# Kernel optimization log

Measured on AMD Instinct MI355X. Metric: run time of the kernel, lower is better.

Reference implementation:

```python
import jax, jax.numpy as jnp
import numpy as np

B, T, C = 8, 2048, 1024
HEAD_SIZE = 64
HEAD_NUM = 0
NUM_HEADS = 16


def setup_inputs() -> dict:
    key = jax.random.key(0)
    k1, k2, k3, k4 = jax.random.split(key, 4)
    x = jax.random.normal(k1, (B, T, C), dtype=jnp.float32)
    s = C ** -0.5  # Linear init scale
    Wq = jax.random.normal(k2, (C, HEAD_SIZE), dtype=jnp.float32) * s
    Wk = jax.random.normal(k3, (C, HEAD_SIZE), dtype=jnp.float32) * s
    Wv = jax.random.normal(k4, (C, HEAD_SIZE), dtype=jnp.float32) * s
    return {"x": x, "Wq": Wq, "Wk": Wk, "Wv": Wv}


def reference(x, Wq, Wk, Wv):
    # single head of self-attention with ALiBi bias + causal mask (dropout in eval mode = identity)
    q = x @ Wq  # [B,T,H]
    k = x @ Wk  # [B,T,H]
    v = x @ Wv  # [B,T,H]
    scale = jnp.float32(HEAD_SIZE) ** -0.5
    t = jnp.arange(T)
    # base_bias[i,j] = j - i, scaled by per-head ALiBi slope
    slope = 2.0 ** (-8.0 * (HEAD_NUM + 1) / NUM_HEADS)
    m = (t[None, :] - t[:, None]).astype(jnp.float32) * slope  # [T,T]
    # note: bias is added BEFORE the 1/sqrt(d) scaling, as in the original
    scores = (jnp.einsum('bqh,bkh->bqk', q, k) + m) * scale  # [B,T,T]
    causal = t[None, :] <= t[:, None]  # [T,T] lower-triangular
    scores = jnp.where(causal, scores, -jnp.inf)
    attn = jax.nn.softmax(scores, axis=-1)
    out = jnp.einsum('bqk,bkh->bqh', attn, v)  # [B,T,H]
    return out
```

## Files before the change

### kernel.cpp

```cpp
#include <hip/hip_runtime.h>
#include <hip/hip_bf16.h>
#include <math.h>

#define B_ 8
#define T_ 2048
#define C_ 1024
#define H_ 64
#define M_ (B_*T_)

typedef __attribute__((ext_vector_type(8))) short bf16x8;
typedef __attribute__((ext_vector_type(4))) float floatx4;

static __device__ __forceinline__ unsigned short f2bf(float f) {
    union { float f; unsigned u; } v; v.f = f;
    unsigned r = v.u + 0x7fffu + ((v.u >> 16) & 1u);
    return (unsigned short)(r >> 16);
}
static __device__ __forceinline__ unsigned short f2bf_fast(float f) {
    union { float f; unsigned u; } v; v.f = f;
    return (unsigned short)((v.u + 0x8000u) >> 16);
}
static __device__ __forceinline__ unsigned pk2h(float lo, float hi) {
    union { float f; unsigned u; } a, b; a.f = lo; b.f = hi;
    return __builtin_amdgcn_perm(b.u + 0x8000u, a.u + 0x8000u, 0x07060302u);
}
static __device__ __forceinline__ bf16x8 cvt8(float4 f0, float4 f1) {
    union { uint4 u; bf16x8 v; } r;
    r.u.x = pk2h(f0.x, f0.y); r.u.y = pk2h(f0.z, f0.w);
    r.u.z = pk2h(f1.x, f1.y); r.u.w = pk2h(f1.z, f1.w);
    return r.v;
}
static __device__ __forceinline__ float fexp2(float x) {
#if defined(__has_builtin)
#if __has_builtin(__builtin_amdgcn_exp2f)
    return __builtin_amdgcn_exp2f(x);
#else
    return exp2f(x);
#endif
#else
    return exp2f(x);
#endif
}

#define MFMA(a,b,c) __builtin_amdgcn_mfma_f32_16x16x32_bf16((a),(b),(c),0,0,0)

__global__ __launch_bounds__(256) void wprep_kernel(
    const float* __restrict__ Wq, const float* __restrict__ Wk,
    const float* __restrict__ Wv, unsigned short* __restrict__ wt2)
{
    const int f    = blockIdx.x * 256 + threadIdx.x;
    const int nt   = f >> 11;
    const int kc   = (f >> 6) & 31;
    const int lane = f & 63;
    const int l15  = lane & 15, quad = lane >> 4;
    const int col  = nt * 16 + l15;
    const float* W = (col < 64) ? Wq : ((col < 128) ? Wk : Wv);
    const int   cw = col & 63;
    const float sc = (col < 64) ? 0.125f : 1.0f;
    unsigned short o[8];
    #pragma unroll
    for (int j = 0; j < 8; j++) {
        const int kk = kc * 32 + quad * 8 + j;
        o[j] = f2bf(W[(size_t)kk * 64 + cw] * sc);
    }
    *(uint4*)&wt2[(size_t)f * 8] = *(const uint4*)o;
}

__global__ __launch_bounds__(256) void qkv_kernel(
    const float* __restrict__ x, const unsigned short* __restrict__ wt2,
    unsigned short* __restrict__ qo, unsigned short* __restrict__ ko,
    unsigned short* __restrict__ vo)
{
    __shared__ __align__(16) unsigned short smem[32 * 200];
    #define XS_(buf) (smem + (buf) * 2304)

    const int t    = threadIdx.x;
    const int w    = t >> 6;
    const int lane = t & 63;
    const int l15  = lane & 15;
    const int quad = lane >> 4;
    const int r0   = blockIdx.x * 32;

    const int srow = t >> 3;
    const int g0   = t & 7;
    const float* xrow = x + (size_t)(r0 + srow) * C_;

    const unsigned short* wb = wt2 + (size_t)(w * 3) * 32 * 512 + lane * 8;

    floatx4 acc[2][3];
    #pragma unroll
    for (int mt = 0; mt < 2; mt++)
        #pragma unroll
        for (int nt = 0; nt < 3; nt++) acc[mt][nt] = (floatx4)(0.0f);

    float4 xA[2], xB[2];
    bf16x8 wcur[6], wnxt[6];

    xA[0] = *(const float4*)(xrow + g0 * 8);
    xA[1] = *(const float4*)(xrow + g0 * 8 + 4);
    xB[0] = *(const float4*)(xrow + 64 + g0 * 8);
    xB[1] = *(const float4*)(xrow + 64 + g0 * 8 + 4);
    #pragma unroll
    for (int nt = 0; nt < 3; nt++)
        #pragma unroll
        for (int ks = 0; ks < 2; ks++)
            wcur[nt * 2 + ks] = *(const bf16x8*)(wb + (size_t)(nt * 32 + ks) * 512);
    *(bf16x8*)(XS_(0) + srow * 72 + g0 * 8) = cvt8(xA[0], xA[1]);
    __syncthreads();

    #define QSTEP(c, Xcur, Xnext, buf)                                         \
    {                                                                          \
        if ((c) < 14) {                                                        \
            const int k2 = ((c) + 2) * 64;                                     \
            Xcur[0] = *(const float4*)(xrow + k2 + g0 * 8);                    \
            Xcur[1] = *(const float4*)(xrow + k2 + g0 * 8 + 4);                \
        }                                                                      \
        if ((c) < 15) {                                                        \
            _Pragma("unroll")                                                  \
            for (int nt = 0; nt < 3; nt++)                                     \
                _Pragma("unroll")                                              \
                for (int ks = 0; ks < 2; ks++)                                 \
                    wnxt[nt * 2 + ks] = *(const bf16x8*)                       \
                        (wb + (size_t)(nt * 32 + 2 * ((c) + 1) + ks) * 512);   \
        }                                                                      \
        _Pragma("unroll")                                                      \
        for (int ks = 0; ks < 2; ks++) {                                       \
            bf16x8 af[2];                                                      \
            _Pragma("unroll")                                                  \
            for (int mt = 0; mt < 2; mt++)                                     \
                af[mt] = *(const bf16x8*)                                      \
                    (XS_(buf) + (mt * 16 + l15) * 72 + ks * 32 + quad * 8);    \
            _Pragma("unroll")                                                  \
            for (int mt = 0; mt < 2; mt++)                                     \
                _Pragma("unroll")                                              \
                for (int nt = 0; nt < 3; nt++)                                 \
                    acc[mt][nt] = MFMA(af[mt], wcur[nt * 2 + ks], acc[mt][nt]);\
        }                                                                      \
        if ((c) < 15) {                                                        \
            *(bf16x8*)(XS_((buf) ^ 1) + srow * 72 + g0 * 8)                    \
                = cvt8(Xnext[0], Xnext[1]);                                    \
            _Pragma("unroll")                                                  \
            for (int i = 0; i < 6; i++) wcur[i] = wnxt[i];                     \
        }                                                                      \
        __syncthreads();                                                       \
    }

    for (int cc = 0; cc < 16; cc += 2) {
        QSTEP(cc,     xA, xB, 0)
        QSTEP(cc + 1, xB, xA, 1)
    }
    #undef QSTEP

    #pragma unroll
    for (int mt = 0; mt < 2; mt++)
        #pragma unroll
        for (int nt = 0; nt < 3; nt++) {
            const int col = w * 48 + nt * 16 + l15;
            #pragma unroll
            for (int r = 0; r < 4; r++)
                smem[(mt * 16 + quad * 4 + r) * 200 + col] = f2bf(acc[mt][nt][r]);
        }
    __syncthreads();

    {
        const int row = t >> 3;
        const int oct = t & 7;
        *(uint4*)&qo[(size_t)(r0 + row) * 64 + oct * 8] =
            *(const uint4*)&smem[row * 200 + oct * 8];
        *(uint4*)&ko[(size_t)(r0 + row) * 64 + oct * 8] =
            *(const uint4*)&smem[row * 200 + 64 + oct * 8];
    }
    {
        const int h = t >> 2, ts = (t & 3) * 8;
        const int bb = r0 >> 11, tt = r0 & 2047;
        unsigned short tmp[8];
        #pragma unroll
        for (int j = 0; j < 8; j++) tmp[j] = smem[(ts + j) * 200 + 128 + h];
        *(uint4*)&vo[((size_t)bb * 64 + h) * 2048 + tt + ts] = *(uint4*)&tmp[0];
    }
    #undef XS_
}

#define L2E 1.4426950408889634f
#define BS2 0.12751743f

__global__ __launch_bounds__(256, 2) void attn_kernel(
    const unsigned short* __restrict__ q,
    const unsigned short* __restrict__ k,
    const unsigned short* __restrict__ vT,
    float* __restrict__ out)
{
    __shared__ __align__(16) unsigned char smem[32768 + 1024];
    unsigned short* pT  = (unsigned short*)smem;
    float*          Omg = (float*)smem;
    float*          mlg = (float*)(smem + 32768);

    const int t    = threadIdx.x;
    const int w    = t >> 6;
    const int lane = t & 63;
    const int l15  = lane & 15;
    const int quad = lane >> 4;
    const int b    = blockIdx.x & 7;
    const int qt   = 63 - (blockIdx.x >> 3);
    const int q0   = qt * 32;
    const size_t kb = (size_t)b * T_ * 64;

    bf16x8 qf[2][2];
    #pragma unroll
    for (int rt = 0; rt < 2; rt++)
        #pragma unroll
        for (int ks = 0; ks < 2; ks++)
            qf[rt][ks] = *(const bf16x8*)
                &q[kb + (size_t)(q0 + rt * 16 + l15) * 64 + ks * 32 + quad * 8];

    floatx4 O[2][4];
    float mrow[2][4], lrow[2][4];
    #pragma unroll
    for (int rt = 0; rt < 2; rt++) {
        #pragma unroll
        for (int nt = 0; nt < 4; nt++) O[rt][nt] = (floatx4)(0.0f);
        #pragma unroll
        for (int r = 0; r < 4; r++) { mrow[rt][r] = -INFINITY; lrow[rt][r] = 0.0f; }
    }

    const int nsteps = (q0 + 32 + 63) >> 6;
    const int ns4    = (nsteps + 3) >> 2;
    const int sBeg   = w * ns4;
    const int sEnd   = min(sBeg + ns4, nsteps);
    unsigned short* pw = pT + w * 32 * 72;

    bf16x8 kf[4][2], vf[4][2];
    #define LOADK(dK, jj0)                                                     \
        { _Pragma("unroll")                                                    \
          for (int nt = 0; nt < 4; nt++)                                       \
              _Pragma("unroll")                                                \
              for (int ks = 0; ks < 2; ks++)                                   \
                  dK[nt][ks] = *(const bf16x8*)                                \
                      &k[kb + (size_t)((jj0) + nt*16 + l15)*64 + ks*32 + quad*8]; }
    #define LOADV(dV, jj0)                                                     \
        { _Pragma("unroll")                                                    \
          for (int nt = 0; nt < 4; nt++)                                       \
              _Pragma("unroll")                                                \
              for (int ks = 0; ks < 2; ks++)                                   \
                  dV[nt][ks] = *(const bf16x8*)                                \
                      &vT[((size_t)b*64 + nt*16 + l15)*2048 + (jj0) + ks*32 + quad*8]; }

    #define SMPART(MASKED)                                                     \
    {                                                                          \
        _Pragma("unroll")                                                      \
        for (int rt = 0; rt < 2; rt++)                                         \
            _Pragma("unroll")                                                  \
            for (int r = 0; r < 4; r++) {                                      \
                float xv[4];                                                   \
                _Pragma("unroll")                                              \
                for (int nt = 0; nt < 4; nt++) {                               \
                    float v2 = fmaf(sc[rt][nt][r], L2E, jn[nt]);               \
                    if (MASKED) {                                              \
                        const int ig = q0 + rt * 16 + quad * 4 + r;            \
                        if (j0 + nt * 16 + l15 > ig) v2 = -INFINITY;           \
                    }                                                          \
                    xv[nt] = v2;                                               \
                }                                                              \
                float mloc = fmaxf(fmaxf(xv[0], xv[1]), fmaxf(xv[2], xv[3]));  \
                _Pragma("unroll")                                              \
                for (int off = 1; off < 16; off <<= 1)                         \
                    mloc = fmaxf(mloc, __shfl_xor(mloc, off));                 \
                const float mnew  = fmaxf(mrow[rt][r], mloc);                  \
                const float alpha = fexp2(mrow[rt][r] - mnew);                 \
                mrow[rt][r] = mnew;                                            \
                float ps = 0.0f;                                               \
                _Pragma("unroll")                                              \
                for (int nt = 0; nt < 4; nt++) {                               \
                    const float p = fexp2(xv[nt] - mnew);                      \
                    ps += p;                                                   \
                    pw[(rt * 16 + quad * 4 + r) * 72 + nt * 16 + l15]          \
                        = f2bf_fast(p);                                        \
                }                                                              \
                lrow[rt][r] = lrow[rt][r] * alpha + ps;                        \
                _Pragma("unroll")                                              \
                for (int nt = 0; nt < 4; nt++) O[rt][nt][r] *= alpha;          \
            }                                                                  \
    }

    if (sBeg < sEnd) LOADK(kf, sBeg * 64)

    for (int s = sBeg; s < sEnd; s++) {
        const int j0 = s * 64;

        floatx4 sc[2][4];
        #pragma unroll
        for (int rt = 0; rt < 2; rt++)
            #pragma unroll
            for (int nt = 0; nt < 4; nt++) {
                floatx4 z = (floatx4)(0.0f);
                z = MFMA(qf[rt][0], kf[nt][0], z);
                z = MFMA(qf[rt][1], kf[nt][1], z);
                sc[rt][nt] = z;
            }

        LOADV(vf, j0)
        bf16x8 kf2[4][2];
        const bool more = (s + 1 < sEnd);
        if (more) LOADK(kf2, (s + 1) * 64)

        const float jb = (float)(j0 + l15) * BS2;
        const float jn[4] = { jb, jb + 16.0f * BS2, jb + 32.0f * BS2,
                              jb + 48.0f * BS2 };
        if (s != nsteps - 1) SMPART(false) else SMPART(true);

        #pragma unroll
        for (int rt = 0; rt < 2; rt++) {
            const bf16x8 pf0 = *(const bf16x8*)&pw[(rt * 16 + l15) * 72 + quad * 8];
            const bf16x8 pf1 = *(const bf16x8*)&pw[(rt * 16 + l15) * 72 + 32 + quad * 8];
            #pragma unroll
            for (int nt = 0; nt < 4; nt++) {
                O[rt][nt] = MFMA(pf0, vf[nt][0], O[rt][nt]);
                O[rt][nt] = MFMA(pf1, vf[nt][1], O[rt][nt]);
            }
        }

        if (more) {
            #pragma unroll
            for (int nt = 0; nt < 4; nt++)
                #pragma unroll
                for (int ks = 0; ks < 2; ks++)
                    kf[nt][ks] = kf2[nt][ks];
        }
    }
    #undef LOADK
    #undef LOADV
    #undef SMPART

    #pragma unroll
    for (int rt = 0; rt < 2; rt++)
        #pragma unroll
        for (int r = 0; r < 4; r++)
            #pragma unroll
            for (int off = 1; off < 16; off <<= 1)
                lrow[rt][r] += __shfl_xor(lrow[rt][r], off);

    __syncthreads();

    #pragma unroll
    for (int rt = 0; rt < 2; rt++)
        #pragma unroll
        for (int nt = 0; nt < 4; nt++)
            #pragma unroll
            for (int r = 0; r < 4; r++)
                Omg[w * 2048 + (rt * 16 + quad * 4 + r) * 64 + nt * 16 + l15]
                    = O[rt][nt][r];
    if (l15 == 0) {
        #pragma unroll
        for (int rt = 0; rt < 2; rt++)
            #pragma unroll
            for (int r = 0; r < 4; r++) {
                mlg[w * 64 + rt * 16 + quad * 4 + r]      = mrow[rt][r];
                mlg[w * 64 + 32 + rt * 16 + quad * 4 + r] = lrow[rt][r];
            }
    }
    __syncthreads();

    {
        const int row = t >> 3;
        const int hq  = (t & 7) << 3;
        float mstar = -INFINITY;
        #pragma unroll
        for (int w2 = 0; w2 < 4; w2++)
            mstar = fmaxf(mstar, mlg[w2 * 64 + row]);
        floatx4 oa0 = (floatx4)(0.0f), oa1 = (floatx4)(0.0f);
        float lsum = 0.0f;
        #pragma unroll
        for (int w2 = 0; w2 < 4; w2++) {
            const float wg = fexp2(mlg[w2 * 64 + row] - mstar);
            lsum += wg * mlg[w2 * 64 + 32 + row];
            oa0 += wg * *(const floatx4*)&Omg[w2 * 2048 + row * 64 + hq];
            oa1 += wg * *(const floatx4*)&Omg[w2 * 2048 + row * 64 + hq + 4];
        }
        const float inv = 1.0f / lsum;
        *(floatx4*)&out[kb + (size_t)(q0 + row) * 64 + hq]     = oa0 * inv;
        *(floatx4*)&out[kb + (size_t)(q0 + row) * 64 + hq + 4] = oa1 * inv;
    }
}

extern "C" void kernel_launch(void* const* d_in, const int* in_sizes, int n_in,
                              void* d_out, int out_size, void* d_ws, size_t ws_size,
                              hipStream_t stream) {
    (void)in_sizes; (void)n_in; (void)out_size; (void)ws_size;
    const float* x  = (const float*)d_in[0];
    const float* Wq = (const float*)d_in[1];
    const float* Wk = (const float*)d_in[2];
    const float* Wv = (const float*)d_in[3];
    float* out = (float*)d_out;

    unsigned short* wt2 = (unsigned short*)d_ws;
    unsigned short* qw  = wt2 + 196608;
    unsigned short* kw  = qw + (size_t)M_ * H_;
    unsigned short* vw  = kw + (size_t)M_ * H_;

    wprep_kernel<<<96, 256, 0, stream>>>(Wq, Wk, Wv, wt2);
    qkv_kernel<<<M_ / 32, 256, 0, stream>>>(x, wt2, qw, kw, vw);
    attn_kernel<<<B_ * 64, 256, 0, stream>>>(qw, kw, vw, out);
}
```

Baseline: 137.3 us.

## Stage full x tile in LDS for QKV and halve attention query tile

The QKV projection now loads and converts the block's entire 32x1024 x tile into LDS up front, in an MFMA-fragment-friendly layout. This removes the per-chunk double buffering and the per-chunk barriers from the inner loop, at the cost of 64KB of LDS per block and less overlap between loads and compute. The attention kernel now uses 16-row query tiles instead of 32, doubling the grid to 1024 blocks. It also shrinks LDS, raises the occupancy hint to 3, pads the P stride to 76, and drops the separate K prefetch registers to lower register pressure. In exchange, each block does less work per K/V load, so global reuse is lower.

```diff
diff --git a/kernel.cpp b/kernel.cpp
--- a/kernel.cpp
+++ b/kernel.cpp
@@ -71,8 +71,7 @@
     unsigned short* __restrict__ qo, unsigned short* __restrict__ ko,
     unsigned short* __restrict__ vo)
 {
-    __shared__ __align__(16) unsigned short smem[32 * 200];
-    #define XS_(buf) (smem + (buf) * 2304)
+    __shared__ __align__(16) unsigned short smem[32768];
 
     const int t    = threadIdx.x;
     const int w    = t >> 6;
@@ -81,9 +80,30 @@
     const int quad = lane >> 4;
     const int r0   = blockIdx.x * 32;
 
-    const int srow = t >> 3;
-    const int g0   = t & 7;
-    const float* xrow = x + (size_t)(r0 + srow) * C_;
+    {
+        const int srow = t >> 3;
+        const int g0   = t & 7;
+        const float* xrow = x + (size_t)(r0 + srow) * C_;
+        const int mt_  = srow >> 4;
+        const int r15_ = srow & 15;
+        const int ks_  = (g0 >> 2) & 1;
+        const int qd_  = g0 & 3;
+        unsigned short* dst = smem + (ks_ * 2 + mt_) * 512 + (qd_ * 16 + r15_) * 8;
+
+        float4 cA0, cA1, cB0, cB1;
+        cA0 = *(const float4*)(xrow + g0 * 8);
+        cA1 = *(const float4*)(xrow + g0 * 8 + 4);
+        #pragma unroll
+        for (int i = 0; i < 16; i++) {
+            if (i < 15) {
+                cB0 = *(const float4*)(xrow + (i + 1) * 64 + g0 * 8);
+                cB1 = *(const float4*)(xrow + (i + 1) * 64 + g0 * 8 + 4);
+            }
+            *(bf16x8*)(dst + i * 2048) = cvt8(cA0, cA1);
+            cA0 = cB0; cA1 = cB1;
+        }
+    }
+    __syncthreads();
 
     const unsigned short* wb = wt2 + (size_t)(w * 3) * 32 * 512 + lane * 8;
 
@@ -93,64 +113,43 @@
         #pragma unroll
         for (int nt = 0; nt < 3; nt++) acc[mt][nt] = (floatx4)(0.0f);
 
-    float4 xA[2], xB[2];
     bf16x8 wcur[6], wnxt[6];
-
-    xA[0] = *(const float4*)(xrow + g0 * 8);
-    xA[1] = *(const float4*)(xrow + g0 * 8 + 4);
-    xB[0] = *(const float4*)(xrow + 64 + g0 * 8);
-    xB[1] = *(const float4*)(xrow + 64 + g0 * 8 + 4);
     #pragma unroll
     for (int nt = 0; nt < 3; nt++)
         #pragma unroll
         for (int ks = 0; ks < 2; ks++)
             wcur[nt * 2 + ks] = *(const bf16x8*)(wb + (size_t)(nt * 32 + ks) * 512);
-    *(bf16x8*)(XS_(0) + srow * 72 + g0 * 8) = cvt8(xA[0], xA[1]);
-    __syncthreads();
-
-    #define QSTEP(c, Xcur, Xnext, buf)                                         \
-    {                                                                          \
-        if ((c) < 14) {                                                        \
-            const int k2 = ((c) + 2) * 64;                                     \
-            Xcur[0] = *(const float4*)(xrow + k2 + g0 * 8);                    \
-            Xcur[1] = *(const float4*)(xrow + k2 + g0 * 8 + 4);                \
-        }                                                                      \
-        if ((c) < 15) {                                                        \
-            _Pragma("unroll")                                                  \
-            for (int nt = 0; nt < 3; nt++)                                     \
-                _Pragma("unroll")                                              \
-                for (int ks = 0; ks < 2; ks++)                                 \
-                    wnxt[nt * 2 + ks] = *(const bf16x8*)                       \
-                        (wb + (size_t)(nt * 32 + 2 * ((c) + 1) + ks) * 512);   \
-        }                                                                      \
-        _Pragma("unroll")                                                      \
-        for (int ks = 0; ks < 2; ks++) {                                       \
-            bf16x8 af[2];                                                      \
-            _Pragma("unroll")                                                  \
-            for (int mt = 0; mt < 2; mt++)                                     \
-                af[mt] = *(const bf16x8*)                                      \
-                    (XS_(buf) + (mt * 16 + l15) * 72 + ks * 32 + quad * 8);    \
-            _Pragma("unroll")                                                  \
-            for (int mt = 0; mt < 2; mt++)                                     \
-                _Pragma("unroll")                                              \
-                for (int nt = 0; nt < 3; nt++)                                 \
-                    acc[mt][nt] = MFMA(af[mt], wcur[nt * 2 + ks], acc[mt][nt]);\
-        }                                                                      \
-        if ((c) < 15) {                                                        \
-            *(bf16x8*)(XS_((buf) ^ 1) + srow * 72 + g0 * 8)                    \
-                = cvt8(Xnext[0], Xnext[1]);                                    \
-            _Pragma("unroll")                                                  \
-            for (int i = 0; i < 6; i++) wcur[i] = wnxt[i];                     \
-        }                                                                      \
-        __syncthreads();                                                       \
-    }
-
-    for (int cc = 0; cc < 16; cc += 2) {
-        QSTEP(cc,     xA, xB, 0)
-        QSTEP(cc + 1, xB, xA, 1)
-    }
-    #undef QSTEP
-
+
+    #pragma unroll 2
+    for (int c = 0; c < 16; c++) {
+        if (c < 15) {
+            #pragma unroll
+            for (int nt = 0; nt < 3; nt++)
+                #pragma unroll
+                for (int ks = 0; ks < 2; ks++)
+                    wnxt[nt * 2 + ks] = *(const bf16x8*)
+                        (wb + (size_t)(nt * 32 + 2 * (c + 1) + ks) * 512);
+        }
+        #pragma unroll
+        for (int ks = 0; ks < 2; ks++) {
+            bf16x8 af[2];
+            #pragma unroll
+            for (int mt = 0; mt < 2; mt++)
+                af[mt] = *(const bf16x8*)
+                    (smem + ((c * 2 + ks) * 2 + mt) * 512 + lane * 8);
+            #pragma unroll
+            for (int mt = 0; mt < 2; mt++)
+                #pragma unroll
+                for (int nt = 0; nt < 3; nt++)
+                    acc[mt][nt] = MFMA(af[mt], wcur[nt * 2 + ks], acc[mt][nt]);
+        }
+        if (c < 15) {
+            #pragma unroll
+            for (int i = 0; i < 6; i++) wcur[i] = wnxt[i];
+        }
+    }
+
+    __syncthreads();
     #pragma unroll
     for (int mt = 0; mt < 2; mt++)
         #pragma unroll
@@ -178,22 +177,22 @@
         for (int j = 0; j < 8; j++) tmp[j] = smem[(ts + j) * 200 + 128 + h];
         *(uint4*)&vo[((size_t)bb * 64 + h) * 2048 + tt + ts] = *(uint4*)&tmp[0];
     }
-    #undef XS_
 }
 
 #define L2E 1.4426950408889634f
 #define BS2 0.12751743f
-
-__global__ __launch_bounds__(256, 2) void attn_kernel(
+#define PSTR 76
+
+__global__ __launch_bounds__(256, 3) void attn_kernel(
     const unsigned short* __restrict__ q,
     const unsigned short* __restrict__ k,
     const unsigned short* __restrict__ vT,
     float* __restrict__ out)
 {
-    __shared__ __align__(16) unsigned char smem[32768 + 1024];
+    __shared__ __align__(16) unsigned char smem[16384 + 512];
     unsigned short* pT  = (unsigned short*)smem;
     float*          Omg = (float*)smem;
-    float*          mlg = (float*)(smem + 32768);
+    float*          mlg = (float*)(smem + 16384);
 
     const int t    = threadIdx.x;
     const int w    = t >> 6;
@@ -201,33 +200,28 @@
     const int l15  = lane & 15;
     const int quad = lane >> 4;
     const int b    = blockIdx.x & 7;
-    const int qt   = 63 - (blockIdx.x >> 3);
-    const int q0   = qt * 32;
+    const int qt   = 127 - (blockIdx.x >> 3);
+    const int q0   = qt * 16;
     const size_t kb = (size_t)b * T_ * 64;
 
-    bf16x8 qf[2][2];
-    #pragma unroll
-    for (int rt = 0; rt < 2; rt++)
-        #pragma unroll
-        for (int ks = 0; ks < 2; ks++)
-            qf[rt][ks] = *(const bf16x8*)
-                &q[kb + (size_t)(q0 + rt * 16 + l15) * 64 + ks * 32 + quad * 8];
-
-    floatx4 O[2][4];
-    float mrow[2][4], lrow[2][4];
-    #pragma unroll
-    for (int rt = 0; rt < 2; rt++) {
-        #pragma unroll
-        for (int nt = 0; nt < 4; nt++) O[rt][nt] = (floatx4)(0.0f);
-        #pragma unroll
-        for (int r = 0; r < 4; r++) { mrow[rt][r] = -INFINITY; lrow[rt][r] = 0.0f; }
-    }
-
-    const int nsteps = (q0 + 32 + 63) >> 6;
+    bf16x8 qf[2];
+    #pragma unroll
+    for (int ks = 0; ks < 2; ks++)
+        qf[ks] = *(const bf16x8*)
+            &q[kb + (size_t)(q0 + l15) * 64 + ks * 32 + quad * 8];
+
+    floatx4 O[4];
+    float mrow[4], lrow[4];
+    #pragma unroll
+    for (int nt = 0; nt < 4; nt++) O[nt] = (floatx4)(0.0f);
+    #pragma unroll
+    for (int r = 0; r < 4; r++) { mrow[r] = -INFINITY; lrow[r] = 0.0f; }
+
+    const int nsteps = (q0 + 16 + 63) >> 6;
     const int ns4    = (nsteps + 3) >> 2;
     const int sBeg   = w * ns4;
     const int sEnd   = min(sBeg + ns4, nsteps);
-    unsigned short* pw = pT + w * 32 * 72;
+    unsigned short* pw = pT + w * 16 * PSTR;
 
     bf16x8 kf[4][2], vf[4][2];
     #define LOADK(dK, jj0)                                                     \
@@ -248,38 +242,35 @@
     #define SMPART(MASKED)                                                     \
     {                                                                          \
         _Pragma("unroll")                                                      \
-        for (int rt = 0; rt < 2; rt++)                                         \
+        for (int r = 0; r < 4; r++) {                                          \
+            float xv[4];                                                       \
             _Pragma("unroll")                                                  \
-            for (int r = 0; r < 4; r++) {                                      \
-                float xv[4];                                                   \
-                _Pragma("unroll")                                              \
-                for (int nt = 0; nt < 4; nt++) {                               \
-                    float v2 = fmaf(sc[rt][nt][r], L2E, jn[nt]);               \
-                    if (MASKED) {                                              \
-                        const int ig = q0 + rt * 16 + quad * 4 + r;            \
-                        if (j0 + nt * 16 + l15 > ig) v2 = -INFINITY;           \
-                    }                                                          \
-                    xv[nt] = v2;                                               \
+            for (int nt = 0; nt < 4; nt++) {                                   \
+                float v2 = fmaf(sc[nt][r], L2E, jn[nt]);                       \
+                if (MASKED) {                                                  \
+                    const int ig = q0 + quad * 4 + r;                          \
+                    if (j0 + nt * 16 + l15 > ig) v2 = -INFINITY;               \
                 }                                                              \
-                float mloc = fmaxf(fmaxf(xv[0], xv[1]), fmaxf(xv[2], xv[3]));  \
-                _Pragma("unroll")                                              \
-                for (int off = 1; off < 16; off <<= 1)                         \
-                    mloc = fmaxf(mloc, __shfl_xor(mloc, off));                 \
-                const float mnew  = fmaxf(mrow[rt][r], mloc);                  \
-                const float alpha = fexp2(mrow[rt][r] - mnew);                 \
-                mrow[rt][r] = mnew;                                            \
-                float ps = 0.0f;                                               \
-                _Pragma("unroll")                                              \
-                for (int nt = 0; nt < 4; nt++) {                               \
-                    const float p = fexp2(xv[nt] - mnew);                      \
-                    ps += p;                                                   \
-                    pw[(rt * 16 + quad * 4 + r) * 72 + nt * 16 + l15]          \
-                        = f2bf_fast(p);                                        \
-                }                                                              \
-                lrow[rt][r] = lrow[rt][r] * alpha + ps;                        \
-                _Pragma("unroll")                                              \
-                for (int nt = 0; nt < 4; nt++) O[rt][nt][r] *= alpha;          \
+                xv[nt] = v2;                                                   \
             }                                                                  \
+            float mloc = fmaxf(fmaxf(xv[0], xv[1]), fmaxf(xv[2], xv[3]));      \
+            _Pragma("unroll")                                                  \
+            for (int off = 1; off < 16; off <<= 1)                             \
+                mloc = fmaxf(mloc, __shfl_xor(mloc, off));                     \
+            const float mnew  = fmaxf(mrow[r], mloc);                          \
+            const float alpha = fexp2(mrow[r] - mnew);                         \
+            mrow[r] = mnew;                                                    \
+            float ps = 0.0f;                                                   \
+            _Pragma("unroll")                                                  \
+            for (int nt = 0; nt < 4; nt++) {                                   \
+                const float p = fexp2(xv[nt] - mnew);                          \
+                ps += p;                                                       \
+                pw[(quad * 4 + r) * PSTR + nt * 16 + l15] = f2bf_fast(p);      \
+            }                                                                  \
+            lrow[r] = lrow[r] * alpha + ps;                                    \
+            _Pragma("unroll")                                                  \
+            for (int nt = 0; nt < 4; nt++) O[nt][r] *= alpha;                  \
+        }                                                                      \
     }
 
     if (sBeg < sEnd) LOADK(kf, sBeg * 64)
@@ -287,44 +278,30 @@
     for (int s = sBeg; s < sEnd; s++) {
         const int j0 = s * 64;
 
-        floatx4 sc[2][4];
-        #pragma unroll
-        for (int rt = 0; rt < 2; rt++)
-            #pragma unroll
-            for (int nt = 0; nt < 4; nt++) {
-                floatx4 z = (floatx4)(0.0f);
-                z = MFMA(qf[rt][0], kf[nt][0], z);
-                z = MFMA(qf[rt][1], kf[nt][1], z);
-                sc[rt][nt] = z;
-            }
+        floatx4 sc[4];
+        #pragma unroll
+        for (int nt = 0; nt < 4; nt++) {
+            floatx4 z = (floatx4)(0.0f);
+            z = MFMA(qf[0], kf[nt][0], z);
+            z = MFMA(qf[1], kf[nt][1], z);
+            sc[nt] = z;
+        }
 
         LOADV(vf, j0)
-        bf16x8 kf2[4][2];
         const bool more = (s + 1 < sEnd);
-        if (more) LOADK(kf2, (s + 1) * 64)
+        if (more) LOADK(kf, (s + 1) * 64)
 
         const float jb = (float)(j0 + l15) * BS2;
         const float jn[4] = { jb, jb + 16.0f * BS2, jb + 32.0f * BS2,
                               jb + 48.0f * BS2 };
         if (s != nsteps - 1) SMPART(false) else SMPART(true);
 
-        #pragma unroll
-        for (int rt = 0; rt < 2; rt++) {
-            const bf16x8 pf0 = *(const bf16x8*)&pw[(rt * 16 + l15) * 72 + quad * 8];
-            const bf16x8 pf1 = *(const bf16x8*)&pw[(rt * 16 + l15) * 72 + 32 + quad * 8];
-            #pragma unroll
-            for (int nt = 0; nt < 4; nt++) {
-                O[rt][nt] = MFMA(pf0, vf[nt][0], O[rt][nt]);
-                O[rt][nt] = MFMA(pf1, vf[nt][1], O[rt][nt]);
-            }
-        }
-
-        if (more) {
-            #pragma unroll
-            for (int nt = 0; nt < 4; nt++)
-                #pragma unroll
-                for (int ks = 0; ks < 2; ks++)
-                    kf[nt][ks] = kf2[nt][ks];
+        const bf16x8 pf0 = *(const bf16x8*)&pw[l15 * PSTR + quad * 8];
+        const bf16x8 pf1 = *(const bf16x8*)&pw[l15 * PSTR + 32 + quad * 8];
+        #pragma unroll
+        for (int nt = 0; nt < 4; nt++) {
+            O[nt] = MFMA(pf0, vf[nt][0], O[nt]);
+            O[nt] = MFMA(pf1, vf[nt][1], O[nt]);
         }
     }
     #undef LOADK
@@ -332,53 +309,43 @@
     #undef SMPART
 
     #pragma unroll
-    for (int rt = 0; rt < 2; rt++)
+    for (int r = 0; r < 4; r++)
+        #pragma unroll
+        for (int off = 1; off < 16; off <<= 1)
+            lrow[r] += __shfl_xor(lrow[r], off);
+
+    __syncthreads();
+
+    #pragma unroll
+    for (int nt = 0; nt < 4; nt++)
         #pragma unroll
         for (int r = 0; r < 4; r++)
-            #pragma unroll
-            for (int off = 1; off < 16; off <<= 1)
-                lrow[rt][r] += __shfl_xor(lrow[rt][r], off);
-
-    __syncthreads();
-
-    #pragma unroll
-    for (int rt = 0; rt < 2; rt++)
-        #pragma unroll
-        for (int nt = 0; nt < 4; nt++)
-            #pragma unroll
-            for (int r = 0; r < 4; r++)
-                Omg[w * 2048 + (rt * 16 + quad * 4 + r) * 64 + nt * 16 + l15]
-                    = O[rt][nt][r];
+            Omg[w * 1024 + (quad * 4 + r) * 64 + nt * 16 + l15] = O[nt][r];
     if (l15 == 0) {
         #pragma unroll
-        for (int rt = 0; rt < 2; rt++)
-            #pragma unroll
-            for (int r = 0; r < 4; r++) {
-                mlg[w * 64 + rt * 16 + quad * 4 + r]      = mrow[rt][r];
-                mlg[w * 64 + 32 + rt * 16 + quad * 4 + r] = lrow[rt][r];
-            }
+        for (int r = 0; r < 4; r++) {
+            mlg[w * 32 + quad * 4 + r]      = mrow[r];
+            mlg[w * 32 + 16 + quad * 4 + r] = lrow[r];
+        }
     }
     __syncthreads();
 
     {
-        const int row = t >> 3;
-        const int hq  = (t & 7) << 3;
+        const int row = t >> 4;
+        const int c4  = (t & 15) << 2;
         float mstar = -INFINITY;
         #pragma unroll
         for (int w2 = 0; w2 < 4; w2++)
-            mstar = fmaxf(mstar, mlg[w2 * 64 + row]);
-        floatx4 oa0 = (floatx4)(0.0f), oa1 = (floatx4)(0.0f);
+            mstar = fmaxf(mstar, mlg[w2 * 32 + row]);
+        floatx4 oa = (floatx4)(0.0f);
         float lsum = 0.0f;
         #pragma unroll
         for (int w2 = 0; w2 < 4; w2++) {
-            const float wg = fexp2(mlg[w2 * 64 + row] - mstar);
-            lsum += wg * mlg[w2 * 64 + 32 + row];
-            oa0 += wg * *(const floatx4*)&Omg[w2 * 2048 + row * 64 + hq];
-            oa1 += wg * *(const floatx4*)&Omg[w2 * 2048 + row * 64 + hq + 4];
-        }
-        const float inv = 1.0f / lsum;
-        *(floatx4*)&out[kb + (size_t)(q0 + row) * 64 + hq]     = oa0 * inv;
-        *(floatx4*)&out[kb + (size_t)(q0 + row) * 64 + hq + 4] = oa1 * inv;
+            const float wg = fexp2(mlg[w2 * 32 + row] - mstar);
+            lsum += wg * mlg[w2 * 32 + 16 + row];
+            oa += wg * *(const floatx4*)&Omg[w2 * 1024 + row * 64 + c4];
+        }
+        *(floatx4*)&out[kb + (size_t)(q0 + row) * 64 + c4] = oa * (1.0f / lsum);
     }
 }
 
@@ -399,5 +366,5 @@
 
     wprep_kernel<<<96, 256, 0, stream>>>(Wq, Wk, Wv, wt2);
     qkv_kernel<<<M_ / 32, 256, 0, stream>>>(x, wt2, qw, kw, vw);
-    attn_kernel<<<B_ * 64, 256, 0, stream>>>(qw, kw, vw, out);
-}
+    attn_kernel<<<B_ * 128, 256, 0, stream>>>(qw, kw, vw, out);
+}
```

New measurement: 143.4 us. 4.4% more time.
